# Kernel optimization log

Hardware: AMD Instinct MI355X
Metric: run time of the kernel (lower is better)

The kernel has to match this reference:

```python
import jax, jax.numpy as jnp
import numpy as np
import math

NUM_HEADS = 16
KEY_SIZE = 64
HIDDEN = 4096
EMBED = 1024
VOCAB = 32000
SEQ = 2048
LAYERS = 4


def rmsnorm(x):
    return x * jax.lax.rsqrt(jnp.mean(x * x, axis=-1, keepdims=True) + 1e-5)


def rope_buffers(seq, d):
    half = d // 2
    i = jnp.arange(d)
    offset = i % half
    scales = jnp.power(10000.0, (-2.0 / d) * offset.astype(jnp.float32))
    m = jnp.arange(seq, dtype=jnp.float32)
    angles = m[:, None] * scales[None, :]  # [S, D]
    cos = jnp.cos(angles)
    sin = jnp.sin(angles)
    sin = jnp.concatenate([-sin[:, :half], sin[:, half:]], axis=-1)
    return cos, sin


def rotate(x, cos, sin):
    # x: [B, H, S, D]; cos/sin: [S, D]
    half = KEY_SIZE // 2
    swapped = jnp.concatenate([x[..., half:], x[..., :half]], axis=-1)
    return cos[None, None] * x + sin[None, None] * swapped


def setup_inputs() -> dict:
    key = jax.random.key(0)
    ks = jax.random.split(key, 7)
    std = 0.02
    return {
        'tokens': jax.random.randint(ks[0], (1, SEQ), 0, VOCAB),
        'table': jax.random.normal(ks[1], (VOCAB, EMBED), jnp.float32) * std,
        'qkv_w': jax.random.normal(ks[2], (LAYERS, EMBED, 3 * NUM_HEADS * KEY_SIZE), jnp.float32) * std,
        'out_w': jax.random.normal(ks[3], (LAYERS, NUM_HEADS * KEY_SIZE, EMBED), jnp.float32) * std,
        'up_w': jax.random.normal(ks[4], (LAYERS, EMBED, 2 * HIDDEN), jnp.float32) * std,
        'down_w': jax.random.normal(ks[5], (LAYERS, HIDDEN, EMBED), jnp.float32) * std,
        'vocab_w': jax.random.normal(ks[6], (EMBED, VOCAB), jnp.float32) * std,
    }


def reference(tokens, table, qkv_w, out_w, up_w, down_w, vocab_w):
    B, S = tokens.shape
    H, D = NUM_HEADS, KEY_SIZE
    # module zeroes embedding row 0 each forward
    table = table.at[0].set(0.0)
    cos, sin = rope_buffers(S, D)
    causal = jnp.tril(jnp.ones((S, S), dtype=bool))  # context_size == S -> pure causal
    emb = table[tokens]  # [B, S, E]
    for l in range(LAYERS):
        # --- self attention ---
        normed = rmsnorm(emb)
        qkv = normed @ qkv_w[l]  # [B, S, 3HD]
        q, k, v = jnp.split(qkv, 3, axis=-1)
        q = q.reshape(B, S, H, D).transpose(0, 2, 1, 3)
        k = k.reshape(B, S, H, D).transpose(0, 2, 1, 3)
        v = v.reshape(B, S, H, D).transpose(0, 2, 1, 3)
        q = rotate(q, cos, sin)
        k = rotate(k, cos, sin)
        attn = jnp.einsum('bhqd,bhkd->bhqk', q, k) / math.sqrt(D)
        attn = jnp.where(causal[None, None], attn, -jnp.inf)
        attn = jax.nn.softmax(attn, axis=-1)
        out = jnp.einsum('bhqk,bhkd->bhqd', attn, v)
        out = out.transpose(0, 2, 1, 3).reshape(B, S, H * D)
        emb = emb + out @ out_w[l]
        # --- SwiGLU FFN ---
        normed = rmsnorm(emb)
        gate_up = normed @ up_w[l]
        gate, up = gate_up[..., :HIDDEN], gate_up[..., HIDDEN:]
        emb = emb + (up * jax.nn.silu(gate)) @ down_w[l]
    emb = rmsnorm(emb)
    logits = emb @ vocab_w  # [B, S, V]
    return logits
```

## Files before the change

kernel.cpp:

```cpp
#include <hip/hip_runtime.h>
#include <hip/hip_bf16.h>

typedef __attribute__((ext_vector_type(8))) short short8;
typedef __attribute__((ext_vector_type(4))) float f32x4;

__device__ __forceinline__ ushort f2bf(float f) {
  uint32_t u = __float_as_uint(f);
  uint32_t r = (u + 0x7FFFu + ((u >> 16) & 1u)) >> 16;
  return (ushort)r;
}
__device__ __forceinline__ float bf2f(ushort u) {
  return __uint_as_float(((uint32_t)u) << 16);
}

__device__ __forceinline__ void gload_lds16(const ushort* g, ushort* l) {
  __builtin_amdgcn_global_load_lds(
      (const __attribute__((address_space(1))) void*)g,
      (__attribute__((address_space(3))) void*)l, 16, 0, 0);
}

__device__ __forceinline__ f32x4 mfma16(short8 a, short8 b, f32x4 c) {
  return __builtin_amdgcn_mfma_f32_16x16x32_bf16(a, b, c, 0, 0, 0);
}

#define BAR() __builtin_amdgcn_s_barrier()
#define WAIT_LGKM()                                        \
  do {                                                     \
    asm volatile("s_waitcnt lgkmcnt(0)" ::: "memory");     \
    __builtin_amdgcn_sched_barrier(0);                     \
  } while (0)
#define WAIT_VM0()                                         \
  do {                                                     \
    asm volatile("s_waitcnt vmcnt(0)" ::: "memory");       \
    __builtin_amdgcn_sched_barrier(0);                     \
  } while (0)

__global__ __launch_bounds__(256)
void transpose_conv_kernel(const float* __restrict__ W, ushort* __restrict__ WT,
                           const int K, const int N, const int mode) {
  const size_t lofs = (size_t)blockIdx.z * K * N;
  W += lofs;
  WT += lofs;
  __shared__ float tile[64][65];
  const int n0 = blockIdx.x * 64;
  const int k0 = blockIdx.y * 64;
  const int t = threadIdx.x;
#pragma unroll
  for (int j = 0; j < 4; ++j) {
    const int idx = j * 1024 + t * 4;
    const int kk = idx >> 6, nn = idx & 63;
    *(float4*)&tile[kk][nn] = *(const float4*)&W[(size_t)(k0 + kk) * N + n0 + nn];
  }
  __syncthreads();
#pragma unroll
  for (int j = 0; j < 4; ++j) {
    const int idx = j * 1024 + t * 4;
    const int nn = idx >> 6, kk = idx & 63;
    int rr = n0 + nn;
    if (mode == 1) rr = (rr < 4096) ? (2 * rr) : (2 * (rr - 4096) + 1);
    ushort4 o;
    o.x = f2bf(tile[kk + 0][nn]);
    o.y = f2bf(tile[kk + 1][nn]);
    o.z = f2bf(tile[kk + 2][nn]);
    o.w = f2bf(tile[kk + 3][nn]);
    *(ushort4*)&WT[(size_t)rr * K + k0 + kk] = o;
  }
}

__global__ __launch_bounds__(256)
void sincos_kernel(float2* __restrict__ cstab) {
  const int idx = blockIdx.x * 256 + threadIdx.x;
  const int s = idx >> 5, o = idx & 31;
  const float freq = exp2f(-0.41524101186092029f * (float)o);
  const float a = (float)s * freq;
  cstab[idx] = make_float2(cosf(a), sinf(a));
}

__global__ __launch_bounds__(256)
void embed_norm_kernel(const int* __restrict__ tokens, const float* __restrict__ table,
                       float* __restrict__ emb, ushort* __restrict__ normed) {
  const int s = blockIdx.x, t = threadIdx.x;
  const int tok = tokens[s];
  float4 v = make_float4(0.f, 0.f, 0.f, 0.f);
  if (tok != 0) v = *(const float4*)&table[(size_t)tok * 1024 + t * 4];
  *(float4*)&emb[(size_t)s * 1024 + t * 4] = v;
  float ss = v.x * v.x + v.y * v.y + v.z * v.z + v.w * v.w;
#pragma unroll
  for (int off = 32; off; off >>= 1) ss += __shfl_xor(ss, off);
  __shared__ float red[4];
  if ((t & 63) == 0) red[t >> 6] = ss;
  __syncthreads();
  const float total = red[0] + red[1] + red[2] + red[3];
  const float sc = rsqrtf(total * (1.f / 1024.f) + 1e-5f);
  ushort4 o;
  o.x = f2bf(v.x * sc); o.y = f2bf(v.y * sc);
  o.z = f2bf(v.z * sc); o.w = f2bf(v.w * sc);
  *(ushort4*)&normed[(size_t)s * 1024 + t * 4] = o;
}

__global__ __launch_bounds__(256)
void rmsnorm_kernel(const float* __restrict__ x, ushort* __restrict__ out) {
  const int row = blockIdx.x, t = threadIdx.x;
  const float4 v = *(const float4*)&x[(size_t)row * 1024 + t * 4];
  float ss = v.x * v.x + v.y * v.y + v.z * v.z + v.w * v.w;
#pragma unroll
  for (int off = 32; off; off >>= 1) ss += __shfl_xor(ss, off);
  __shared__ float red[4];
  if ((t & 63) == 0) red[t >> 6] = ss;
  __syncthreads();
  const float total = red[0] + red[1] + red[2] + red[3];
  const float sc = rsqrtf(total * (1.f / 1024.f) + 1e-5f);
  ushort4 o;
  o.x = f2bf(v.x * sc); o.y = f2bf(v.y * sc);
  o.z = f2bf(v.z * sc); o.w = f2bf(v.w * sc);
  *(ushort4*)&out[(size_t)row * 1024 + t * 4] = o;
}

__global__ __launch_bounds__(256)
void vtrans_kernel(const ushort* __restrict__ vh, ushort* __restrict__ vt) {
  __shared__ ushort tv[64][68];
  const int h = blockIdx.y;
  const int s0 = blockIdx.x * 64;
  const int t = threadIdx.x;
#pragma unroll
  for (int j = 0; j < 4; ++j) {
    const int idx = j * 1024 + t * 4;
    const int s = idx >> 6, d4 = idx & 63;
    *(ushort4*)&tv[s][d4] = *(const ushort4*)&vh[((size_t)h * 2048 + s0 + s) * 64 + d4];
  }
  __syncthreads();
#pragma unroll
  for (int j = 0; j < 4; ++j) {
    const int idx = j * 1024 + t * 4;
    const int d = idx >> 6, s4 = idx & 63;
    ushort4 ov;
    ov.x = tv[s4 + 0][d];
    ov.y = tv[s4 + 1][d];
    ov.z = tv[s4 + 2][d];
    ov.w = tv[s4 + 3][d];
    *(ushort4*)&vt[((size_t)h * 64 + d) * 2048 + s0 + s4] = ov;
  }
}

__global__ __launch_bounds__(256)
void attn_mfma_kernel(const ushort* __restrict__ qh, const ushort* __restrict__ kh,
                      const ushort* __restrict__ vt, ushort* __restrict__ attn_out) {
  __shared__ ushort sQ[64 * 64];
  __shared__ ushort sK[64 * 64];
  __shared__ ushort sV[64 * 64];
  __shared__ ushort sP[4][1024];
  const int h = blockIdx.y;
  const int bx = blockIdx.x;
  const int qt = (h < 8) ? bx : 31 - bx;
  const int i0 = qt * 64;
  const int tid = threadIdx.x;
  const int w = tid >> 6, lane = tid & 63;
  const int llo = lane & 15, lhi = lane >> 4;
  const int lr = lane >> 3, lc = lane & 7;
  const ushort* qg = qh + ((size_t)h * 2048 + i0) * 64;
  const ushort* kg = kh + (size_t)h * 2048 * 64;
  const ushort* vg = vt + (size_t)h * 64 * 2048;

#pragma unroll
  for (int j = 0; j < 2; ++j) {
    const int r0 = (w * 2 + j) * 8;
    const int row = r0 + lr;
    gload_lds16(qg + (size_t)row * 64 + ((lc ^ (row & 7)) * 8), &sQ[r0 * 64]);
  }
  __syncthreads();
  const int qrow = w * 16 + llo;
  const short8 qf0 = *(const short8*)&sQ[qrow * 64 + ((lhi ^ (qrow & 7)) * 8)];
  const short8 qf1 = *(const short8*)&sQ[qrow * 64 + (((4 + lhi) ^ (qrow & 7)) * 8)];

  float m = -1e30f, lsum = 0.f;
  f32x4 o[4] = {};
  const int nch = qt + 1;
  for (int cb = 0; cb < nch; ++cb) {
    const int kb = cb * 64;
    __syncthreads();
#pragma unroll
    for (int j = 0; j < 2; ++j) {
      const int r0 = (w * 2 + j) * 8;
      const int row = r0 + lr;
      gload_lds16(kg + (size_t)(kb + row) * 64 + ((lc ^ (row & 7)) * 8), &sK[r0 * 64]);
      gload_lds16(vg + (size_t)row * 2048 + kb + ((lc ^ (row & 7)) * 8), &sV[r0 * 64]);
    }
    __syncthreads();

    f32x4 st[4] = {};
#pragma unroll
    for (int ck = 0; ck < 2; ++ck) {
      const short8 qf = ck ? qf1 : qf0;
#pragma unroll
      for (int f = 0; f < 4; ++f) {
        const int key = f * 16 + llo;
        const short8 kf = *(const short8*)&sK[key * 64 + (((ck * 4 + lhi) ^ (key & 7)) * 8)];
        st[f] = mfma16(kf, qf, st[f]);
      }
    }

    float pv[4][4];
    const bool diag = (kb == i0);
#pragma unroll
    for (int f = 0; f < 4; ++f)
#pragma unroll
      for (int r = 0; r < 4; ++r) {
        float x = st[f][r] * 0.125f;
        if (diag && (f * 16 + lhi * 4 + r) > qrow) x = -1e30f;
        pv[f][r] = x;
      }
    float mr = pv[0][0];
#pragma unroll
    for (int f = 0; f < 4; ++f)
#pragma unroll
      for (int r = 0; r < 4; ++r) mr = fmaxf(mr, pv[f][r]);
    mr = fmaxf(mr, __shfl_xor(mr, 16));
    mr = fmaxf(mr, __shfl_xor(mr, 32));
    const float mnew = fmaxf(m, mr);
    const float scale = __expf(m - mnew);
    m = mnew;
    float rs = 0.f;
#pragma unroll
    for (int f = 0; f < 4; ++f)
#pragma unroll
      for (int r = 0; r < 4; ++r) {
        const float p = __expf(pv[f][r] - mnew);
        pv[f][r] = p;
        rs += p;
      }
    rs += __shfl_xor(rs, 16);
    rs += __shfl_xor(rs, 32);
    lsum = lsum * scale + rs;
    float scr[4];
#pragma unroll
    for (int r = 0; r < 4; ++r) scr[r] = __shfl(scale, lhi * 4 + r);
#pragma unroll
    for (int nn = 0; nn < 4; ++nn)
#pragma unroll
      for (int r = 0; r < 4; ++r) o[nn][r] *= scr[r];

    ushort* pw = sP[w];
#pragma unroll
    for (int f = 0; f < 4; ++f) {
      uint2 pk;
      pk.x = (uint)f2bf(pv[f][0]) | ((uint)f2bf(pv[f][1]) << 16);
      pk.y = (uint)f2bf(pv[f][2]) | ((uint)f2bf(pv[f][3]) << 16);
      *(uint2*)&pw[llo * 64 + ((f * 16 + lhi * 4) ^ ((llo & 7) << 3))] = pk;
    }
    const short8 pf0 = *(const short8*)&pw[llo * 64 + ((lhi ^ (llo & 7)) * 8)];
    const short8 pf1 = *(const short8*)&pw[llo * 64 + (((4 + lhi) ^ (llo & 7)) * 8)];

#pragma unroll
    for (int ck = 0; ck < 2; ++ck) {
      const short8 pf = ck ? pf1 : pf0;
#pragma unroll
      for (int nn = 0; nn < 4; ++nn) {
        const int drow = nn * 16 + llo;
        const short8 vf = *(const short8*)&sV[drow * 64 + (((ck * 4 + lhi) ^ (drow & 7)) * 8)];
        o[nn] = mfma16(pf, vf, o[nn]);
      }
    }
  }

  const float inv = 1.f / lsum;
  float invr[4];
#pragma unroll
  for (int r = 0; r < 4; ++r) invr[r] = __shfl(inv, lhi * 4 + r);
#pragma unroll
  for (int nn = 0; nn < 4; ++nn)
#pragma unroll
    for (int r = 0; r < 4; ++r) {
      const int row = i0 + w * 16 + lhi * 4 + r;
      attn_out[(size_t)row * 1024 + h * 64 + nn * 16 + llo] = f2bf(o[nn][r] * invr[r]);
    }
}

template <int BM, int BN, int EPI>
__global__ __launch_bounds__(256)
void gemm_bt_kernel(const ushort* __restrict__ A, const ushort* __restrict__ BT,
                    const float* __restrict__ addend, void* __restrict__ Cout,
                    const int M, const int N, const int K) {
  constexpr int WM = BM / 2, WN = BN / 2;
  constexpr int FM = WM / 16, FN = WN / 16;
  constexpr int CHA = BM / 16, CHB = BN / 16;
  __shared__ ushort sA[BM * 32];
  __shared__ ushort sB[BN * 32];
  const int bm0 = blockIdx.y * BM;
  const int bn0 = blockIdx.x * BN;
  const int tid = threadIdx.x;
  const int wid = tid >> 6;
  const int lane = tid & 63;
  const int wr = wid >> 1, wc = wid & 1;
  const int lhi = lane >> 4, llo = lane & 15;
  f32x4 acc[FM][FN] = {};
  for (int kt = 0; kt < K; kt += 32) {
#pragma unroll
    for (int c2 = 0; c2 < CHA / 4; ++c2) {
      const int ch = c2 * 4 + wid;
      const int e = ch * 512 + lane * 8;
      gload_lds16(A + (size_t)(bm0 + (e >> 5)) * K + kt + (e & 31), sA + ch * 512);
    }
#pragma unroll
    for (int c2 = 0; c2 < CHB / 4; ++c2) {
      const int ch = c2 * 4 + wid;
      const int e = ch * 512 + lane * 8;
      gload_lds16(BT + (size_t)(bn0 + (e >> 5)) * K + kt + (e & 31), sB + ch * 512);
    }
    __syncthreads();
    short8 aF[FM], bF[FN];
#pragma unroll
    for (int mm = 0; mm < FM; ++mm)
      aF[mm] = *(const short8*)&sA[(wr * WM + mm * 16 + llo) * 32 + lhi * 8];
#pragma unroll
    for (int nn = 0; nn < FN; ++nn)
      bF[nn] = *(const short8*)&sB[(wc * WN + nn * 16 + llo) * 32 + lhi * 8];
#pragma unroll
    for (int mm = 0; mm < FM; ++mm)
#pragma unroll
      for (int nn = 0; nn < FN; ++nn)
        acc[mm][nn] = __builtin_amdgcn_mfma_f32_16x16x32_bf16(aF[mm], bF[nn],
                                                              acc[mm][nn], 0, 0, 0);
    __syncthreads();
  }
#pragma unroll
  for (int mm = 0; mm < FM; ++mm) {
#pragma unroll
    for (int nn = 0; nn < FN; ++nn) {
      const int col = bn0 + wc * WN + nn * 16 + llo;
#pragma unroll
      for (int r = 0; r < 4; ++r) {
        const int row = bm0 + wr * WM + mm * 16 + lhi * 4 + r;
        float v = acc[mm][nn][r];
        if constexpr (EPI == 1) v += addend[(size_t)row * N + col];
        ((float*)Cout)[(size_t)row * N + col] = v;
      }
    }
  }
}

__global__ __launch_bounds__(256)
void gemm_qkv_kernel(const ushort* __restrict__ A, const ushort* __restrict__ BT,
                     const float2* __restrict__ cstab, ushort* __restrict__ qh,
                     ushort* __restrict__ kh, ushort* __restrict__ vh, const int K) {
  constexpr int BM = 64, BN = 128, WM = 32, WN = 64, FM = 2, FN = 4;
  constexpr int CHA = BM / 16, CHB = BN / 16;
  __shared__ ushort sA[BM * 32];
  __shared__ ushort sB[BN * 32];
  const int bm0 = blockIdx.y * BM;
  const int bn0 = blockIdx.x * BN;
  const int tid = threadIdx.x;
  const int wid = tid >> 6;
  const int lane = tid & 63;
  const int wr = wid >> 1, wc = wid & 1;
  const int lhi = lane >> 4, llo = lane & 15;
  f32x4 acc[FM][FN] = {};
  for (int kt = 0; kt < K; kt += 32) {
#pragma unroll
    for (int c2 = 0; c2 < CHA / 4; ++c2) {
      const int ch = c2 * 4 + wid;
      const int e = ch * 512 + lane * 8;
      gload_lds16(A + (size_t)(bm0 + (e >> 5)) * K + kt + (e & 31), sA + ch * 512);
    }
#pragma unroll
    for (int c2 = 0; c2 < CHB / 4; ++c2) {
      const int ch = c2 * 4 + wid;
      const int e = ch * 512 + lane * 8;
      gload_lds16(BT + (size_t)(bn0 + (e >> 5)) * K + kt + (e & 31), sB + ch * 512);
    }
    __syncthreads();
    short8 aF[FM], bF[FN];
#pragma unroll
    for (int mm = 0; mm < FM; ++mm)
      aF[mm] = *(const short8*)&sA[(wr * WM + mm * 16 + llo) * 32 + lhi * 8];
#pragma unroll
    for (int nn = 0; nn < FN; ++nn)
      bF[nn] = *(const short8*)&sB[(wc * WN + nn * 16 + llo) * 32 + lhi * 8];
#pragma unroll
    for (int mm = 0; mm < FM; ++mm)
#pragma unroll
      for (int nn = 0; nn < FN; ++nn)
        acc[mm][nn] = mfma16(aF[mm], bF[nn], acc[mm][nn]);
    __syncthreads();
  }
#pragma unroll
  for (int mm = 0; mm < FM; ++mm) {
#pragma unroll
    for (int nn = 0; nn < FN; ++nn) {
      const int col = bn0 + wc * WN + nn * 16 + llo;
      const int part = col >> 10;
      const int hcol = col & 1023;
      const int h = hcol >> 6;
      const int d = hcol & 63;
      const int off = d & 31;
#pragma unroll
      for (int r = 0; r < 4; ++r) {
        const int row = bm0 + wr * WM + mm * 16 + lhi * 4 + r;
        const float v = acc[mm][nn][r];
        const size_t ho = ((size_t)h * 2048 + row) * 64 + d;
        if (part == 2) {
          vh[ho] = f2bf(v);
        } else {
          const float pt = acc[mm][nn ^ 2][r];
          const float2 cn = cstab[row * 32 + off];
          const float si = (d < 32) ? -cn.y : cn.y;
          const ushort o = f2bf(cn.x * v + si * pt);
          if (part == 0) qh[ho] = o; else kh[ho] = o;
        }
      }
    }
  }
}

#define LDA_(MH)                                                              \
  {                                                                           \
    _Pragma("unroll") for (int mm = 0; mm < 4; ++mm) {                        \
      const int row = wr * 128 + ((MH) * 4 + mm) * 16 + llo;                  \
      _Pragma("unroll") for (int ks = 0; ks < 2; ++ks)                        \
          aF[mm][ks] = *(const short8*)&cA[row * 64 +                         \
                          (((ks * 4 + lhi) ^ (row & 7)) * 8)];                \
    }                                                                         \
  }
#define LDB_(NH)                                                              \
  {                                                                           \
    _Pragma("unroll") for (int nn = 0; nn < 2; ++nn) {                        \
      const int row = wc * 64 + ((NH) * 2 + nn) * 16 + llo;                   \
      _Pragma("unroll") for (int ks = 0; ks < 2; ++ks)                        \
          bF[nn][ks] = *(const short8*)&cB[row * 64 +                         \
                          (((ks * 4 + lhi) ^ (row & 7)) * 8)];                \
    }                                                                         \
  }
#define MFMAQ_(MH, NH)                                                        \
  {                                                                           \
    __builtin_amdgcn_s_setprio(1);                                            \
    _Pragma("unroll") for (int mm = 0; mm < 4; ++mm)                          \
        _Pragma("unroll") for (int nn = 0; nn < 2; ++nn)                      \
            _Pragma("unroll") for (int ks = 0; ks < 2; ++ks)                  \
                acc[(MH) * 4 + mm][(NH) * 2 + nn] =                           \
                    mfma16(aF[mm][ks], bF[nn][ks],                            \
                           acc[(MH) * 4 + mm][(NH) * 2 + nn]);                \
    __builtin_amdgcn_s_setprio(0);                                            \
  }

template <int EPI>
__global__ __launch_bounds__(512, 2)
void gemm8_kernel(const ushort* __restrict__ A, const ushort* __restrict__ BT,
                  void* __restrict__ Cout,
                  const int M, const int N, const int K, const int nby) {
  extern __shared__ ushort smem[];
  const int nwg = gridDim.x;
  const int cpx = nwg >> 3;
  int id = blockIdx.x;
  id = (id & 7) * cpx + (id >> 3);
  const int by = id % nby, bx = id / nby;
  const int bm0 = by * 256, bn0 = bx * 256;
  const int tid = threadIdx.x;
  const int wid = tid >> 6, lane = tid & 63;
  const int wr = wid >> 2, wc = wid & 3;
  const int llo = lane & 15, lhi = lane >> 4;
  const ushort* gA = A + (size_t)bm0 * K;
  const ushort* gB = BT + (size_t)bn0 * K;

  auto stage = [&](const ushort* g, ushort* dst, int kt) {
#pragma unroll
    for (int i = 0; i < 4; ++i) {
      const int chunk = i * 512 + wid * 64 + lane;
      const int row = chunk >> 3, c = chunk & 7;
      gload_lds16(g + (size_t)row * K + kt + ((c ^ (row & 7)) * 8),
                  dst + (size_t)(i * 512 + wid * 64) * 8);
    }
  };

  f32x4 acc[8][4] = {};
  short8 aF[4][2];
  short8 bF[2][2];

  stage(gA, smem, 0);
  stage(gB, smem + 16384, 0);
  WAIT_VM0();
  BAR();

  const int nt = K >> 6;
  for (int t = 0; t < nt; ++t) {
    const int cur = t & 1;
    ushort* cA = smem + cur * 32768;
    ushort* cB = cA + 16384;
    ushort* nA = smem + (cur ^ 1) * 32768;
    ushort* nB = nA + 16384;
    const bool pf = (t + 1 < nt);
    LDA_(0); LDB_(0);
    if (pf) { stage(gA, nA, (t + 1) * 64); stage(gB, nB, (t + 1) * 64); }
    BAR(); WAIT_LGKM();
    MFMAQ_(0, 0);
    BAR();
    LDB_(1);
    BAR(); WAIT_LGKM();
    MFMAQ_(0, 1);
    BAR();
    LDA_(1);
    BAR(); WAIT_LGKM();
    MFMAQ_(1, 1);
    BAR();
    LDB_(0);
    BAR(); WAIT_LGKM();
    MFMAQ_(1, 0);
    if (pf) WAIT_VM0();
    BAR();
  }

#pragma unroll
  for (int m = 0; m < 8; ++m) {
#pragma unroll
    for (int n = 0; n < 4; ++n) {
      const int col = bn0 + wc * 64 + n * 16 + llo;
#pragma unroll
      for (int r = 0; r < 4; ++r) {
        const int row = bm0 + wr * 128 + m * 16 + lhi * 4 + r;
        float v = acc[m][n][r];
        if constexpr (EPI == 3) {
          const float other = __shfl_xor(v, 1);
          if ((llo & 1) == 0) {
            const float gate = v, up = other;
            const float hh = up * gate / (1.f + expf(-gate));
            ((ushort*)Cout)[(size_t)row * (N >> 1) + (col >> 1)] = f2bf(hh);
          }
        } else {
          ((float*)Cout)[(size_t)row * N + col] = v;
        }
      }
    }
  }
}

extern "C" void kernel_launch(void* const* d_in, const int* in_sizes, int n_in,
                              void* d_out, int out_size, void* d_ws, size_t ws_size,
                              hipStream_t stream) {
  const int* tokens    = (const int*)d_in[0];
  const float* table   = (const float*)d_in[1];
  const float* qkv_w   = (const float*)d_in[2];
  const float* out_w   = (const float*)d_in[3];
  const float* up_w    = (const float*)d_in[4];
  const float* down_w  = (const float*)d_in[5];
  const float* vocab_w = (const float*)d_in[6];
  float* logits = (float*)d_out;

  constexpr int G8_LDS = 131072;
  hipFuncSetAttribute(reinterpret_cast<const void*>(&gemm8_kernel<0>),
                      hipFuncAttributeMaxDynamicSharedMemorySize, G8_LDS);
  hipFuncSetAttribute(reinterpret_cast<const void*>(&gemm8_kernel<3>),
                      hipFuncAttributeMaxDynamicSharedMemorySize, G8_LDS);

  char* p = (char*)d_ws;
  auto alloc = [&](size_t bytes) {
    char* r = p;
    p += (bytes + 255) & ~(size_t)255;
    return r;
  };
  float*  emb    = (float*)alloc(2048ull * 1024 * 4);
  ushort* normed = (ushort*)alloc(2048ull * 1024 * 2);
  float2* cstab  = (float2*)alloc(2048ull * 32 * 8);
  ushort* qhb    = (ushort*)alloc(16ull * 2048 * 64 * 2);
  ushort* khb    = (ushort*)alloc(16ull * 2048 * 64 * 2);
  ushort* vhb    = (ushort*)alloc(16ull * 2048 * 64 * 2);
  ushort* vtb    = (ushort*)alloc(16ull * 64 * 2048 * 2);
  ushort* attno  = (ushort*)alloc(2048ull * 1024 * 2);
  ushort* hbuf   = (ushort*)alloc(2048ull * 4096 * 2);
  ushort* qkvT   = (ushort*)alloc(4ull * 3072 * 1024 * 2);
  ushort* outT   = (ushort*)alloc(4ull * 1024 * 1024 * 2);
  ushort* upT    = (ushort*)alloc(4ull * 8192 * 1024 * 2);
  ushort* downT  = (ushort*)alloc(4ull * 1024 * 4096 * 2);
  ushort* vocabT = (ushort*)alloc(32000ull * 1024 * 2);

  transpose_conv_kernel<<<dim3(3072 / 64, 1024 / 64, 4), 256, 0, stream>>>(
      qkv_w, qkvT, 1024, 3072, 0);
  transpose_conv_kernel<<<dim3(1024 / 64, 1024 / 64, 4), 256, 0, stream>>>(
      out_w, outT, 1024, 1024, 0);
  transpose_conv_kernel<<<dim3(8192 / 64, 1024 / 64, 4), 256, 0, stream>>>(
      up_w, upT, 1024, 8192, 1);
  transpose_conv_kernel<<<dim3(1024 / 64, 4096 / 64, 4), 256, 0, stream>>>(
      down_w, downT, 4096, 1024, 0);
  transpose_conv_kernel<<<dim3(32000 / 64, 1024 / 64, 1), 256, 0, stream>>>(
      vocab_w, vocabT, 1024, 32000, 0);
  sincos_kernel<<<256, 256, 0, stream>>>(cstab);

  embed_norm_kernel<<<2048, 256, 0, stream>>>(tokens, table, emb, normed);

  for (int l = 0; l < 4; ++l) {
    if (l > 0) rmsnorm_kernel<<<2048, 256, 0, stream>>>(emb, normed);
    gemm_qkv_kernel<<<dim3(3072 / 128, 2048 / 64), 256, 0, stream>>>(
        normed, qkvT + (size_t)l * 3072 * 1024, cstab, qhb, khb, vhb, 1024);
    vtrans_kernel<<<dim3(32, 16), 256, 0, stream>>>(vhb, vtb);
    attn_mfma_kernel<<<dim3(32, 16), 256, 0, stream>>>(qhb, khb, vtb, attno);
    gemm_bt_kernel<64, 128, 1><<<dim3(1024 / 128, 2048 / 64), 256, 0, stream>>>(
        attno, outT + (size_t)l * 1024 * 1024, emb, emb, 2048, 1024, 1024);
    rmsnorm_kernel<<<2048, 256, 0, stream>>>(emb, normed);
    gemm8_kernel<3><<<(8192 / 256) * (2048 / 256), 512, G8_LDS, stream>>>(
        normed, upT + (size_t)l * 8192 * 1024, hbuf, 2048, 8192, 1024, 2048 / 256);
    gemm_bt_kernel<64, 128, 1><<<dim3(1024 / 128, 2048 / 64), 256, 0, stream>>>(
        hbuf, downT + (size_t)l * 1024 * 4096, emb, emb, 2048, 1024, 4096);
  }
  rmsnorm_kernel<<<2048, 256, 0, stream>>>(emb, normed);
  gemm8_kernel<0><<<(32000 / 256) * (2048 / 256), 512, G8_LDS, stream>>>(
      normed, vocabT, logits, 2048, 32000, 1024, 2048 / 256);
}
```

Measured before the change: 1.316 ms.

## Add triple-buffered pipelined GEMM kernel for the vocabulary projection

Measured after the change: 1.317 ms. Within noise of the previous version (+0.1%).

```diff
diff --git a/kernel.cpp b/kernel.cpp
--- a/kernel.cpp
+++ b/kernel.cpp
@@ -32,6 +32,11 @@
 #define WAIT_VM0()                                         \
   do {                                                     \
     asm volatile("s_waitcnt vmcnt(0)" ::: "memory");       \
+    __builtin_amdgcn_sched_barrier(0);                     \
+  } while (0)
+#define WAIT_VM4()                                         \
+  do {                                                     \
+    asm volatile("s_waitcnt vmcnt(4)" ::: "memory");       \
     __builtin_amdgcn_sched_barrier(0);                     \
   } while (0)
 
@@ -531,6 +536,111 @@
   }
 }
 
+template <int EPI>
+__global__ __launch_bounds__(512, 2)
+void gemm8p_kernel(const ushort* __restrict__ A, const ushort* __restrict__ BT,
+                   void* __restrict__ Cout,
+                   const int M, const int N, const int K, const int nby) {
+  extern __shared__ ushort smem[];
+  const int nwg = gridDim.x;
+  const int cpx = nwg >> 3;
+  int id = blockIdx.x;
+  id = (id & 7) * cpx + (id >> 3);
+  const int by = id % nby, bx = id / nby;
+  const int bm0 = by * 256, bn0 = bx * 256;
+  const int tid = threadIdx.x;
+  const int wid = tid >> 6, lane = tid & 63;
+  const int wr = wid >> 2, wc = wid & 3;
+  const int llo = lane & 15, lhi = lane >> 4;
+  const ushort* gA = A + (size_t)bm0 * K;
+  const ushort* gB = BT + (size_t)bn0 * K;
+
+  auto stage = [&](ushort* dst, int kt) {
+#pragma unroll
+    for (int i = 0; i < 2; ++i) {
+      const int cb = i * 512 + wid * 64;
+      const int ch = cb + lane;
+      const int row = ch >> 2, c = ch & 3;
+      gload_lds16(gA + (size_t)row * K + kt + ((c ^ ((row >> 1) & 3)) * 8),
+                  dst + (size_t)cb * 8);
+    }
+#pragma unroll
+    for (int i = 0; i < 2; ++i) {
+      const int cb = i * 512 + wid * 64;
+      const int ch = cb + lane;
+      const int row = ch >> 2, c = ch & 3;
+      gload_lds16(gB + (size_t)row * K + kt + ((c ^ ((row >> 1) & 3)) * 8),
+                  dst + 8192 + (size_t)cb * 8);
+    }
+  };
+
+  f32x4 acc[8][4] = {};
+  short8 aF[4], bF[4];
+
+  const int nt = K >> 5;
+  stage(smem, 0);
+  stage(smem + 16384, 32);
+  WAIT_VM4();
+  BAR();
+
+  int cs = 0;
+  for (int t = 0; t < nt; ++t) {
+    ushort* cA = smem + cs * 16384;
+    ushort* cB = cA + 8192;
+    int ss = cs + 2; if (ss >= 3) ss -= 3;
+    const bool pf2 = (t + 2 < nt);
+    if (pf2) stage(smem + ss * 16384, (t + 2) * 32);
+#pragma unroll
+    for (int mm = 0; mm < 4; ++mm) {
+      const int row = wr * 128 + mm * 16 + llo;
+      aF[mm] = *(const short8*)&cA[row * 32 + ((lhi ^ ((row >> 1) & 3)) * 8)];
+    }
+#pragma unroll
+    for (int nn = 0; nn < 4; ++nn) {
+      const int row = wc * 64 + nn * 16 + llo;
+      bF[nn] = *(const short8*)&cB[row * 32 + ((lhi ^ ((row >> 1) & 3)) * 8)];
+    }
+    BAR(); WAIT_LGKM();
+    __builtin_amdgcn_s_setprio(1);
+#pragma unroll
+    for (int mm = 0; mm < 4; ++mm)
+#pragma unroll
+      for (int nn = 0; nn < 4; ++nn)
+        acc[mm][nn] = mfma16(aF[mm], bF[nn], acc[mm][nn]);
+    __builtin_amdgcn_s_setprio(0);
+    BAR();
+#pragma unroll
+    for (int mm = 0; mm < 4; ++mm) {
+      const int row = wr * 128 + (mm + 4) * 16 + llo;
+      aF[mm] = *(const short8*)&cA[row * 32 + ((lhi ^ ((row >> 1) & 3)) * 8)];
+    }
+    BAR(); WAIT_LGKM();
+    __builtin_amdgcn_s_setprio(1);
+#pragma unroll
+    for (int mm = 0; mm < 4; ++mm)
+#pragma unroll
+      for (int nn = 0; nn < 4; ++nn)
+        acc[mm + 4][nn] = mfma16(aF[mm], bF[nn], acc[mm + 4][nn]);
+    __builtin_amdgcn_s_setprio(0);
+    if (pf2) { WAIT_VM4(); } else { WAIT_VM0(); }
+    BAR();
+    ++cs; if (cs == 3) cs = 0;
+  }
+
+#pragma unroll
+  for (int m = 0; m < 8; ++m) {
+#pragma unroll
+    for (int n = 0; n < 4; ++n) {
+      const int col = bn0 + wc * 64 + n * 16 + llo;
+#pragma unroll
+      for (int r = 0; r < 4; ++r) {
+        const int row = bm0 + wr * 128 + m * 16 + lhi * 4 + r;
+        ((float*)Cout)[(size_t)row * N + col] = acc[m][n][r];
+      }
+    }
+  }
+}
+
 extern "C" void kernel_launch(void* const* d_in, const int* in_sizes, int n_in,
                               void* d_out, int out_size, void* d_ws, size_t ws_size,
                               hipStream_t stream) {
@@ -544,10 +654,11 @@
   float* logits = (float*)d_out;
 
   constexpr int G8_LDS = 131072;
-  hipFuncSetAttribute(reinterpret_cast<const void*>(&gemm8_kernel<0>),
-                      hipFuncAttributeMaxDynamicSharedMemorySize, G8_LDS);
+  constexpr int G8P_LDS = 98304;
   hipFuncSetAttribute(reinterpret_cast<const void*>(&gemm8_kernel<3>),
                       hipFuncAttributeMaxDynamicSharedMemorySize, G8_LDS);
+  hipFuncSetAttribute(reinterpret_cast<const void*>(&gemm8p_kernel<0>),
+                      hipFuncAttributeMaxDynamicSharedMemorySize, G8P_LDS);
 
   char* p = (char*)d_ws;
   auto alloc = [&](size_t bytes) {
@@ -599,6 +710,6 @@
         hbuf, downT + (size_t)l * 1024 * 4096, emb, emb, 2048, 1024, 4096);
   }
   rmsnorm_kernel<<<2048, 256, 0, stream>>>(emb, normed);
-  gemm8_kernel<0><<<(32000 / 256) * (2048 / 256), 512, G8_LDS, stream>>>(
+  gemm8p_kernel<0><<<(32000 / 256) * (2048 / 256), 512, G8P_LDS, stream>>>(
       normed, vocabT, logits, 2048, 32000, 1024, 2048 / 256);
 }
```
